# Performance work log

Measured on AMD Instinct MI355X. Metric: run time of the kernel, lower is better.

## Reference

```python
import jax, jax.numpy as jnp
import numpy as np

B, C, W, H, HID = 8, 512, 64, 32, 256
G = 5 * HID  # gates: i, f_left, f_up, o, candidate
EPS = 1e-5


def setup_inputs() -> dict:
    key = jax.random.key(0)
    ks = jax.random.split(key, 7)
    s_in = 1.0 / np.sqrt(C)
    s_h = 1.0 / np.sqrt(HID)
    return {
        "x": jax.random.normal(ks[0], (B, C, W, H), dtype=jnp.float32),
        "Wx": jax.random.normal(ks[1], (C, G), dtype=jnp.float32) * s_in,
        "Wh1": jax.random.normal(ks[2], (HID, G), dtype=jnp.float32) * s_h,  # left neighbor
        "Wh2": jax.random.normal(ks[3], (HID, G), dtype=jnp.float32) * s_h,  # up neighbor
        "b": jnp.zeros((G,), dtype=jnp.float32),
        "gamma": jnp.ones((HID,), dtype=jnp.float32),
        "beta": jnp.zeros((HID,), dtype=jnp.float32),
    }


def mdlstm(x, Wx, Wh1, Wh2, b):
    # x: (B, C, W, H). Precompute input projection once (big GEMM).
    xp = jnp.einsum('bcwh,cg->whbg', x, Wx) + b  # (W, H, B, G)
    z = jnp.zeros((B, HID), x.dtype)
    zrow = jnp.zeros((H, B, HID), x.dtype)

    def col_step(carry, inp):
        h_l, c_l = carry                 # left-neighbor state/cell (B, HID)
        xg, h_u, c_u = inp               # precomputed input gates + up-neighbor
        g = xg + h_l @ Wh1 + h_u @ Wh2   # (B, G)
        i, f1, f2, o, cand = jnp.split(g, 5, axis=-1)
        i = jax.nn.sigmoid(i)
        f1 = jax.nn.sigmoid(f1)
        f2 = jax.nn.sigmoid(f2)
        o = jax.nn.sigmoid(o)
        c = i * jnp.tanh(cand) + f1 * c_l + f2 * c_u
        h = o * jnp.tanh(c)
        return (h, c), (h, c)

    def row_step(prev, xp_w):
        h_up_row, c_up_row = prev        # previous width-row, each (H, B, HID)
        _, (h_row, c_row) = jax.lax.scan(col_step, (z, z), (xp_w, h_up_row, c_up_row))
        return (h_row, c_row), (h_row, c_row)

    _, (h_all, c_all) = jax.lax.scan(row_step, (zrow, zrow), xp)  # (W, H, B, HID)
    state = jnp.transpose(h_all, (2, 3, 0, 1))  # (B, HID, W, H)
    cell = jnp.transpose(c_all, (2, 3, 0, 1))
    return state, cell


def reference(x, Wx, Wh1, Wh2, b, gamma, beta):
    state, cell = mdlstm(x, Wx, Wh1, Wh2, b)
    # BatchNorm2d (training-mode batch statistics) over (N, W, H) per channel
    mean = state.mean(axis=(0, 2, 3), keepdims=True)
    var = state.var(axis=(0, 2, 3), keepdims=True)
    xn = (state - mean) * jax.lax.rsqrt(var + EPS)
    out = jnp.tanh(xn * gamma[None, :, None, None] + beta[None, :, None, None])
    return (out, (state, cell))
```

## Files before the change

kernel.cpp:

```cpp
#include <hip/hip_runtime.h>
#include <math.h>

#define B_ 8
#define C_ 512
#define W_ 64
#define H_ 32
#define HID_ 256
#define G_ 1280
#define WH_ (W_*H_)
#define CELL_STRIDE (B_*HID_)
#define SENT 0xFFFFFFFFu

typedef float v4f __attribute__((ext_vector_type(4)));

__device__ __forceinline__ float sigmoidf_(float x) {
    return 1.0f / (1.0f + __expf(-x));
}

__device__ __forceinline__ float tanhf_(float x) {
    float ax = fabsf(x);
    float e = __expf(-2.0f * ax);
    float t = (1.0f - e) / (1.0f + e);
    return copysignf(t, x);
}

__device__ __forceinline__ void stg_byp1(float* p, float v) {
    asm volatile("global_store_dword %0, %1, off sc0 sc1" :: "v"(p), "v"(v) : "memory");
}
__device__ __forceinline__ void ldg2_byp(const unsigned* p0, const unsigned* p1,
                                         unsigned& a, unsigned& b) {
    asm volatile("global_load_dword %0, %2, off sc0 sc1\n\t"
                 "global_load_dword %1, %3, off sc0 sc1\n\t"
                 "s_waitcnt vmcnt(0)"
                 : "=&v"(a), "=&v"(b)
                 : "v"(p0), "v"(p1)
                 : "memory");
}

__device__ __forceinline__ bool ok4(v4f v) {
    return (__float_as_uint(v.x) != SENT) & (__float_as_uint(v.y) != SENT) &
           (__float_as_uint(v.z) != SENT) & (__float_as_uint(v.w) != SENT);
}

__global__ __launch_bounds__(256) void k_transpose_x(const float* __restrict__ x,
                                                     float* __restrict__ xT) {
    __shared__ float tile[64][65];
    int bc0 = blockIdx.x * 64;
    int wh0 = blockIdx.y * 64;
    int xcol = threadIdx.x & 63;
    int yrow = threadIdx.x >> 6;
    for (int yy = yrow; yy < 64; yy += 4)
        tile[yy][xcol] = x[(size_t)(bc0 + yy) * WH_ + wh0 + xcol];
    __syncthreads();
    for (int yy = yrow; yy < 64; yy += 4)
        xT[(size_t)(wh0 + yy) * (B_*C_) + bc0 + xcol] = tile[xcol][yy];
}

#define BM 64
#define BN 128
#define BK 32
#define AS_STRIDE 68
#define BS_STRIDE 132

__global__ __launch_bounds__(256) void k_xproj(const float* __restrict__ xT,
                                               const float* __restrict__ Wx,
                                               const float* __restrict__ bias,
                                               float* __restrict__ xp) {
    __shared__ float As[BK * AS_STRIDE];
    __shared__ float Bs[BK * BS_STRIDE];

    int bid = blockIdx.x;
    int xcd = bid & 7;
    int slot = bid >> 3;
    int mt = xcd * 32 + slot / 10;
    int nt = slot % 10;
    int m0 = mt * BM, n0 = nt * BN;
    int tid = threadIdx.x;

    int tm  = (tid >> 5) * 8;
    int tn4 = (tid & 31) * 4;

    float4 acc[8];
#pragma unroll
    for (int i = 0; i < 8; ++i) { acc[i].x = acc[i].y = acc[i].z = acc[i].w = 0.f; }

    int ar = tid >> 2, aq = tid & 3;
    int br = tid >> 3, bq = tid & 7;

    for (int kc = 0; kc < C_; kc += BK) {
        float4 av0 = *(const float4*)(xT + (size_t)(m0 + ar) * C_ + kc + aq * 4);
        float4 av1 = *(const float4*)(xT + (size_t)(m0 + ar) * C_ + kc + (aq + 4) * 4);
        float4 bv[4];
#pragma unroll
        for (int s = 0; s < 4; ++s)
            bv[s] = *(const float4*)(Wx + (size_t)(kc + br) * G_ + n0 + (bq + 8 * s) * 4);

        __syncthreads();
        As[(aq * 4 + 0) * AS_STRIDE + ar] = av0.x;
        As[(aq * 4 + 1) * AS_STRIDE + ar] = av0.y;
        As[(aq * 4 + 2) * AS_STRIDE + ar] = av0.z;
        As[(aq * 4 + 3) * AS_STRIDE + ar] = av0.w;
        As[((aq + 4) * 4 + 0) * AS_STRIDE + ar] = av1.x;
        As[((aq + 4) * 4 + 1) * AS_STRIDE + ar] = av1.y;
        As[((aq + 4) * 4 + 2) * AS_STRIDE + ar] = av1.z;
        As[((aq + 4) * 4 + 3) * AS_STRIDE + ar] = av1.w;
#pragma unroll
        for (int s = 0; s < 4; ++s)
            *(float4*)&Bs[br * BS_STRIDE + (bq + 8 * s) * 4] = bv[s];
        __syncthreads();

#pragma unroll
        for (int k = 0; k < BK; ++k) {
            float4 a0 = *(const float4*)&As[k * AS_STRIDE + tm];
            float4 a1 = *(const float4*)&As[k * AS_STRIDE + tm + 4];
            float4 b0 = *(const float4*)&Bs[k * BS_STRIDE + tn4];
            float am[8] = {a0.x, a0.y, a0.z, a0.w, a1.x, a1.y, a1.z, a1.w};
#pragma unroll
            for (int i = 0; i < 8; ++i) {
                acc[i].x += am[i] * b0.x;
                acc[i].y += am[i] * b0.y;
                acc[i].z += am[i] * b0.z;
                acc[i].w += am[i] * b0.w;
            }
        }
    }

    float4 bb = *(const float4*)(bias + n0 + tn4);
#pragma unroll
    for (int i = 0; i < 8; ++i) {
        float4 o;
        o.x = acc[i].x + bb.x; o.y = acc[i].y + bb.y;
        o.z = acc[i].z + bb.z; o.w = acc[i].w + bb.w;
        *(float4*)(xp + (size_t)(m0 + tm + i) * G_ + n0 + tn4) = o;
    }
}

#define NT 32
#define NWV 8
#define GPS (NWV*160 + 8)

__global__ __launch_bounds__(512, 2) void k_scan(const float* __restrict__ xp,
                                                 const float* __restrict__ Wh1,
                                                 const float* __restrict__ Wh2,
                                                 float* __restrict__ hbuf,
                                                 float* __restrict__ cbuf) {
    __shared__ float hs[2][B_ * HID_];
    __shared__ float gp[B_ * GPS];

    int w0b = blockIdx.x >> 3;
    int nt  = blockIdx.x & 7;
    int n0  = nt * NT;
    int tid = threadIdx.x;

    int kq  = tid >> 5;
    int c0  = tid & 31;
    int sel = kq >> 3;
    int kk0 = (kq & 7) * 32;
    const float* Wm = sel ? Wh2 : Wh1;
    const float* hbase = &hs[sel][0];
    int wv = tid >> 6;
    bool lo32 = (tid & 63) < 32;

    float wr[5][32];
#pragma unroll
    for (int g = 0; g < 5; ++g)
#pragma unroll
        for (int k = 0; k < 32; ++k)
            wr[g][k] = Wm[(size_t)(kk0 + k) * G_ + g * 256 + n0 + c0];

    int b2 = tid >> 5, nn2 = tid & 31;
    bool cok = (tid < 256);
    int xob = b2 * G_ + n0 + nn2;
    int co  = b2 * HID_ + n0 + nn2;
    int gr  = b2 * GPS + nn2;
    int gwb = wv * 160 + c0;

    for (int rr = 0; rr < 2; ++rr) {
        int w = w0b + rr * 32;
        float creg = 0.f;
        for (int h = 0; h < H_; ++h) {
            int wh = w * H_ + h;

            float xpre[5];
            if (cok) {
                const float* xrow = xp + (size_t)wh * (B_ * G_) + xob;
#pragma unroll
                for (int g = 0; g < 5; ++g) xpre[g] = xrow[g * 256];
            }

            bool vl = (h > 0), vu = (w > 0);
            const float* pl = vl ? hbuf + (size_t)(wh - 1)  * CELL_STRIDE + tid * 4 : hbuf;
            const float* pu = vu ? hbuf + (size_t)(wh - H_) * CELL_STRIDE + tid * 4 : hbuf;
            const float* pc = (vu && cok) ? cbuf + (size_t)(wh - H_) * CELL_STRIDE + co : cbuf;

            if ((tid & 63) == 0) {
                if (vl | vu) {
                    for (;;) {
                        unsigned a, bvv;
                        ldg2_byp((const unsigned*)pl, (const unsigned*)pu, a, bvv);
                        if ((((!vl)) | (a != SENT)) & (((!vu)) | (bvv != SENT))) break;
                        __builtin_amdgcn_s_sleep(2);
                    }
                }
            }

            v4f l0 = {0.f, 0.f, 0.f, 0.f};
            v4f u0 = {0.f, 0.f, 0.f, 0.f};
            float cu = 0.f;
            bool needl = vl, needu = vu, needc = vu && cok;
            for (;;) {
                v4f tl, tu; float tc;
                asm volatile(
                    "global_load_dwordx4 %0, %3, off sc0 sc1\n\t"
                    "global_load_dwordx4 %1, %4, off sc0 sc1\n\t"
                    "global_load_dword %2, %5, off sc0 sc1\n\t"
                    "s_waitcnt vmcnt(0)"
                    : "=&v"(tl), "=&v"(tu), "=&v"(tc)
                    : "v"(pl), "v"(pu), "v"(pc)
                    : "memory");
                if (needl & ok4(tl)) { l0 = tl; needl = false; }
                if (needu & ok4(tu)) { u0 = tu; needu = false; }
                if (needc & (__float_as_uint(tc) != SENT)) { cu = tc; needc = false; }
                if (__ballot(needl | needu | needc) == 0) break;
                __builtin_amdgcn_s_sleep(1);
            }
            ((v4f*)hs[0])[tid] = l0;
            ((v4f*)hs[1])[tid] = u0;
            __syncthreads();

            float acc[5][8];
#pragma unroll
            for (int g = 0; g < 5; ++g)
#pragma unroll
                for (int b = 0; b < 8; ++b) acc[g][b] = 0.f;

#pragma unroll
            for (int k4 = 0; k4 < 8; ++k4) {
#pragma unroll
                for (int b = 0; b < 8; ++b) {
                    float4 hv = *(const float4*)&hbase[b * HID_ + kk0 + k4 * 4];
#pragma unroll
                    for (int g = 0; g < 5; ++g) {
                        acc[g][b] += hv.x * wr[g][k4 * 4 + 0];
                        acc[g][b] += hv.y * wr[g][k4 * 4 + 1];
                        acc[g][b] += hv.z * wr[g][k4 * 4 + 2];
                        acc[g][b] += hv.w * wr[g][k4 * 4 + 3];
                    }
                }
            }

#pragma unroll
            for (int v = 0; v < 20; ++v) {
                const int ia = v, ib = v + 20;
                float xa = acc[ia >> 3][ia & 7], ya = xa;
                float xb = acc[ib >> 3][ib & 7], yb = xb;
                asm("v_permlane32_swap_b32 %0, %1" : "+v"(xa), "+v"(ya));
                asm("v_permlane32_swap_b32 %0, %1" : "+v"(xb), "+v"(yb));
                float sa = xa + ya;
                float sb = xb + yb;
                float val = lo32 ? sa : sb;
                const int offA = (ia & 7) * GPS + (ia >> 3) * 32;
                const int offB = (ib & 7) * GPS + (ib >> 3) * 32;
                gp[gwb + (lo32 ? offA : offB)] = val;
            }
            __syncthreads();

            if (cok) {
                float gv[5];
#pragma unroll
                for (int g = 0; g < 5; ++g) {
                    float s = xpre[g];
#pragma unroll
                    for (int q = 0; q < NWV; ++q)
                        s += gp[gr + q * 160 + g * 32];
                    gv[g] = s;
                }
                float iv = sigmoidf_(gv[0]);
                float f1 = sigmoidf_(gv[1]);
                float f2 = sigmoidf_(gv[2]);
                float ov = sigmoidf_(gv[3]);
                float cd = tanhf_(gv[4]);
                float cv = iv * cd + f1 * creg + f2 * cu;
                float hh = ov * tanhf_(cv);
                creg = cv;
                stg_byp1(cbuf + (size_t)wh * CELL_STRIDE + co, cv);
                stg_byp1(hbuf + (size_t)wh * CELL_STRIDE + co, hh);
            }
        }
    }
}

__global__ __launch_bounds__(256) void k_stats(const float* __restrict__ hbuf,
                                               float* __restrict__ ssum,
                                               float* __restrict__ ssq) {
    int t = threadIdx.x;
    size_t r0 = (size_t)blockIdx.x * 64;
    float s = 0.f, q = 0.f;
    for (int r = 0; r < 64; ++r) {
        float v = hbuf[(r0 + r) * HID_ + t];
        s += v; q += v * v;
    }
    atomicAdd(&ssum[t], s);
    atomicAdd(&ssq[t], q);
}

__global__ void k_finstats(const float* __restrict__ ssum, const float* __restrict__ ssq,
                           float* __restrict__ mean, float* __restrict__ rinv) {
    int t = threadIdx.x;
    const float inv_n = 1.0f / 16384.0f;
    float m = ssum[t] * inv_n;
    float v = ssq[t] * inv_n - m * m;
    mean[t] = m;
    rinv[t] = rsqrtf(v + 1e-5f);
}

__global__ __launch_bounds__(256) void k_out(const float* __restrict__ hbuf,
                                             const float* __restrict__ cbuf,
                                             const float* __restrict__ mean,
                                             const float* __restrict__ rinv,
                                             const float* __restrict__ gamma,
                                             const float* __restrict__ beta,
                                             float* __restrict__ outp) {
    __shared__ float tile[64][65];
    int bi = blockIdx.x;
    int b = bi >> 7;
    int rem = bi & 127;
    int wh0 = (rem >> 2) * 64;
    int n0 = (rem & 3) * 64;
    int xcol = threadIdx.x & 63;
    int yrow = threadIdx.x >> 6;

    float* out0   = outp;
    float* state0 = outp + (size_t)B_ * HID_ * WH_;
    float* cell0  = state0 + (size_t)B_ * HID_ * WH_;

    for (int yy = yrow; yy < 64; yy += 4)
        tile[yy][xcol] = hbuf[((size_t)(wh0 + yy) * B_ + b) * HID_ + n0 + xcol];
    __syncthreads();
    for (int yy = yrow; yy < 64; yy += 4) {
        int n = n0 + yy;
        float sv = tile[xcol][yy];
        size_t oidx = ((size_t)b * HID_ + n) * WH_ + wh0 + xcol;
        state0[oidx] = sv;
        float xn = (sv - mean[n]) * rinv[n];
        out0[oidx] = tanhf_(xn * gamma[n] + beta[n]);
    }
    __syncthreads();

    for (int yy = yrow; yy < 64; yy += 4)
        tile[yy][xcol] = cbuf[((size_t)(wh0 + yy) * B_ + b) * HID_ + n0 + xcol];
    __syncthreads();

    for (int yy = yrow; yy < 64; yy += 4) {
        int n = n0 + yy;
        size_t oidx = ((size_t)b * HID_ + n) * WH_ + wh0 + xcol;
        cell0[oidx] = tile[xcol][yy];
    }
}

extern "C" void kernel_launch(void* const* d_in, const int* in_sizes, int n_in,
                              void* d_out, int out_size, void* d_ws, size_t ws_size,
                              hipStream_t stream) {
    const float* x     = (const float*)d_in[0];
    const float* Wx    = (const float*)d_in[1];
    const float* Wh1   = (const float*)d_in[2];
    const float* Wh2   = (const float*)d_in[3];
    const float* bias  = (const float*)d_in[4];
    const float* gamma = (const float*)d_in[5];
    const float* beta  = (const float*)d_in[6];
    float* out = (float*)d_out;
    float* ws  = (float*)d_ws;

    float* xp   = ws;
    float* xT   = ws + 20971520;
    float* hbuf = xT;
    float* cbuf = xT + 4194304;
    float* ssum = ws + 29360128;
    float* ssq  = ssum + 256;
    float* mean = ssum + 512;
    float* rinv = ssum + 768;

    k_transpose_x<<<dim3(64, 32), 256, 0, stream>>>(x, xT);
    k_xproj<<<2560, 256, 0, stream>>>(xT, Wx, bias, xp);

    hipMemsetAsync(ssum, 0, 1024 * sizeof(float), stream);
    hipMemsetAsync(hbuf, 0xFF, (size_t)8388608 * sizeof(float), stream);

    k_scan<<<256, 512, 0, stream>>>(xp, Wh1, Wh2, hbuf, cbuf);

    k_stats<<<256, 256, 0, stream>>>(hbuf, ssum, ssq);
    k_finstats<<<1, 256, 0, stream>>>(ssum, ssq, mean, rinv);
    k_out<<<8 * 32 * 4, 256, 0, stream>>>(hbuf, cbuf, mean, rinv, gamma, beta, out);
}
```

Before: 1.025 ms.

## Run input projection GEMM on bf16 MFMA with split-precision hi/lo operands

```diff
diff --git a/kernel.cpp b/kernel.cpp
--- a/kernel.cpp
+++ b/kernel.cpp
@@ -12,6 +12,8 @@
 #define SENT 0xFFFFFFFFu
 
 typedef float v4f __attribute__((ext_vector_type(4)));
+typedef __attribute__((ext_vector_type(8))) short bf16x8;
+typedef __attribute__((ext_vector_type(4))) float f32x4;
 
 __device__ __forceinline__ float sigmoidf_(float x) {
     return 1.0f / (1.0f + __expf(-x));
@@ -22,6 +24,15 @@
     float e = __expf(-2.0f * ax);
     float t = (1.0f - e) / (1.0f + e);
     return copysignf(t, x);
+}
+
+__device__ __forceinline__ unsigned short f2bf(float f) {
+    unsigned u = __float_as_uint(f);
+    u = u + 0x7FFFu + ((u >> 16) & 1u);
+    return (unsigned short)(u >> 16);
+}
+__device__ __forceinline__ float bf2f(unsigned short h) {
+    return __uint_as_float(((unsigned)h) << 16);
 }
 
 __device__ __forceinline__ void stg_byp1(float* p, float v) {
@@ -43,7 +54,8 @@
 }
 
 __global__ __launch_bounds__(256) void k_transpose_x(const float* __restrict__ x,
-                                                     float* __restrict__ xT) {
+                                                     unsigned short* __restrict__ xTh,
+                                                     unsigned short* __restrict__ xTl) {
     __shared__ float tile[64][65];
     int bc0 = blockIdx.x * 64;
     int wh0 = blockIdx.y * 64;
@@ -52,86 +64,129 @@
     for (int yy = yrow; yy < 64; yy += 4)
         tile[yy][xcol] = x[(size_t)(bc0 + yy) * WH_ + wh0 + xcol];
     __syncthreads();
+    for (int yy = yrow; yy < 64; yy += 4) {
+        float v = tile[xcol][yy];
+        unsigned short hi = f2bf(v);
+        unsigned short lo = f2bf(v - bf2f(hi));
+        size_t idx = (size_t)(wh0 + yy) * (B_*C_) + bc0 + xcol;
+        xTh[idx] = hi;
+        xTl[idx] = lo;
+    }
+}
+
+__global__ __launch_bounds__(256) void k_wxT(const float* __restrict__ Wx,
+                                             unsigned short* __restrict__ WxTh,
+                                             unsigned short* __restrict__ WxTl) {
+    __shared__ float tile[64][65];
+    int n0 = blockIdx.x * 64;
+    int k0 = blockIdx.y * 64;
+    int xcol = threadIdx.x & 63;
+    int yrow = threadIdx.x >> 6;
     for (int yy = yrow; yy < 64; yy += 4)
-        xT[(size_t)(wh0 + yy) * (B_*C_) + bc0 + xcol] = tile[xcol][yy];
-}
-
-#define BM 64
-#define BN 128
-#define BK 32
-#define AS_STRIDE 68
-#define BS_STRIDE 132
-
-__global__ __launch_bounds__(256) void k_xproj(const float* __restrict__ xT,
-                                               const float* __restrict__ Wx,
-                                               const float* __restrict__ bias,
-                                               float* __restrict__ xp) {
-    __shared__ float As[BK * AS_STRIDE];
-    __shared__ float Bs[BK * BS_STRIDE];
+        tile[yy][xcol] = Wx[(size_t)(k0 + yy) * G_ + n0 + xcol];
+    __syncthreads();
+    for (int yy = yrow; yy < 64; yy += 4) {
+        float v = tile[xcol][yy];
+        unsigned short hi = f2bf(v);
+        unsigned short lo = f2bf(v - bf2f(hi));
+        size_t idx = (size_t)(n0 + yy) * C_ + k0 + xcol;
+        WxTh[idx] = hi;
+        WxTl[idx] = lo;
+    }
+}
+
+#define XAS 40
+
+__global__ __launch_bounds__(256) void k_xproj_mfma(const unsigned short* __restrict__ xTh,
+                                                    const unsigned short* __restrict__ xTl,
+                                                    const unsigned short* __restrict__ WxTh,
+                                                    const unsigned short* __restrict__ WxTl,
+                                                    const float* __restrict__ bias,
+                                                    float* __restrict__ xp) {
+    __shared__ unsigned short Ash[128 * XAS];
+    __shared__ unsigned short Asl[128 * XAS];
+    __shared__ unsigned short Bsh[128 * XAS];
+    __shared__ unsigned short Bsl[128 * XAS];
 
     int bid = blockIdx.x;
-    int xcd = bid & 7;
-    int slot = bid >> 3;
-    int mt = xcd * 32 + slot / 10;
-    int nt = slot % 10;
-    int m0 = mt * BM, n0 = nt * BN;
+    int nt2 = bid % 10;
+    int mt  = bid / 10;
+    int m0 = mt * 128, n0 = nt2 * 128;
     int tid = threadIdx.x;
-
-    int tm  = (tid >> 5) * 8;
-    int tn4 = (tid & 31) * 4;
-
-    float4 acc[8];
-#pragma unroll
-    for (int i = 0; i < 8; ++i) { acc[i].x = acc[i].y = acc[i].z = acc[i].w = 0.f; }
-
-    int ar = tid >> 2, aq = tid & 3;
-    int br = tid >> 3, bq = tid & 7;
-
-    for (int kc = 0; kc < C_; kc += BK) {
-        float4 av0 = *(const float4*)(xT + (size_t)(m0 + ar) * C_ + kc + aq * 4);
-        float4 av1 = *(const float4*)(xT + (size_t)(m0 + ar) * C_ + kc + (aq + 4) * 4);
-        float4 bv[4];
-#pragma unroll
-        for (int s = 0; s < 4; ++s)
-            bv[s] = *(const float4*)(Wx + (size_t)(kc + br) * G_ + n0 + (bq + 8 * s) * 4);
-
+    int lane = tid & 63;
+    int wave = tid >> 6;
+    int wm = (wave >> 1) * 64;
+    int wn = (wave & 1) * 64;
+    int r16 = lane & 15;
+    int kg  = lane >> 4;
+
+    int srow = tid >> 1;
+    int sh   = (tid & 1) * 16;
+
+    f32x4 acc[4][4];
+#pragma unroll
+    for (int i = 0; i < 4; ++i)
+#pragma unroll
+        for (int j = 0; j < 4; ++j)
+            acc[i][j] = (f32x4)0.f;
+
+    const unsigned short* agh = xTh  + (size_t)(m0 + srow) * C_ + sh;
+    const unsigned short* agl = xTl  + (size_t)(m0 + srow) * C_ + sh;
+    const unsigned short* bgh = WxTh + (size_t)(n0 + srow) * C_ + sh;
+    const unsigned short* bgl = WxTl + (size_t)(n0 + srow) * C_ + sh;
+
+    for (int kc = 0; kc < C_; kc += 32) {
+        uint4 ah0 = *(const uint4*)(agh + kc);
+        uint4 ah1 = *(const uint4*)(agh + kc + 8);
+        uint4 al0 = *(const uint4*)(agl + kc);
+        uint4 al1 = *(const uint4*)(agl + kc + 8);
+        uint4 bh0 = *(const uint4*)(bgh + kc);
+        uint4 bh1 = *(const uint4*)(bgh + kc + 8);
+        uint4 bl0 = *(const uint4*)(bgl + kc);
+        uint4 bl1 = *(const uint4*)(bgl + kc + 8);
         __syncthreads();
-        As[(aq * 4 + 0) * AS_STRIDE + ar] = av0.x;
-        As[(aq * 4 + 1) * AS_STRIDE + ar] = av0.y;
-        As[(aq * 4 + 2) * AS_STRIDE + ar] = av0.z;
-        As[(aq * 4 + 3) * AS_STRIDE + ar] = av0.w;
-        As[((aq + 4) * 4 + 0) * AS_STRIDE + ar] = av1.x;
-        As[((aq + 4) * 4 + 1) * AS_STRIDE + ar] = av1.y;
-        As[((aq + 4) * 4 + 2) * AS_STRIDE + ar] = av1.z;
-        As[((aq + 4) * 4 + 3) * AS_STRIDE + ar] = av1.w;
-#pragma unroll
-        for (int s = 0; s < 4; ++s)
-            *(float4*)&Bs[br * BS_STRIDE + (bq + 8 * s) * 4] = bv[s];
+        *(uint4*)&Ash[srow * XAS + sh]     = ah0;
+        *(uint4*)&Ash[srow * XAS + sh + 8] = ah1;
+        *(uint4*)&Asl[srow * XAS + sh]     = al0;
+        *(uint4*)&Asl[srow * XAS + sh + 8] = al1;
+        *(uint4*)&Bsh[srow * XAS + sh]     = bh0;
+        *(uint4*)&Bsh[srow * XAS + sh + 8] = bh1;
+        *(uint4*)&Bsl[srow * XAS + sh]     = bl0;
+        *(uint4*)&Bsl[srow * XAS + sh + 8] = bl1;
         __syncthreads();
 
-#pragma unroll
-        for (int k = 0; k < BK; ++k) {
-            float4 a0 = *(const float4*)&As[k * AS_STRIDE + tm];
-            float4 a1 = *(const float4*)&As[k * AS_STRIDE + tm + 4];
-            float4 b0 = *(const float4*)&Bs[k * BS_STRIDE + tn4];
-            float am[8] = {a0.x, a0.y, a0.z, a0.w, a1.x, a1.y, a1.z, a1.w};
-#pragma unroll
-            for (int i = 0; i < 8; ++i) {
-                acc[i].x += am[i] * b0.x;
-                acc[i].y += am[i] * b0.y;
-                acc[i].z += am[i] * b0.z;
-                acc[i].w += am[i] * b0.w;
-            }
+        bf16x8 afh[4], afl[4], bfh[4], bfl[4];
+#pragma unroll
+        for (int i = 0; i < 4; ++i) {
+            afh[i] = *(const bf16x8*)&Ash[(wm + i * 16 + r16) * XAS + kg * 8];
+            afl[i] = *(const bf16x8*)&Asl[(wm + i * 16 + r16) * XAS + kg * 8];
         }
-    }
-
-    float4 bb = *(const float4*)(bias + n0 + tn4);
-#pragma unroll
-    for (int i = 0; i < 8; ++i) {
-        float4 o;
-        o.x = acc[i].x + bb.x; o.y = acc[i].y + bb.y;
-        o.z = acc[i].z + bb.z; o.w = acc[i].w + bb.w;
-        *(float4*)(xp + (size_t)(m0 + tm + i) * G_ + n0 + tn4) = o;
+#pragma unroll
+        for (int j = 0; j < 4; ++j) {
+            bfh[j] = *(const bf16x8*)&Bsh[(wn + j * 16 + r16) * XAS + kg * 8];
+            bfl[j] = *(const bf16x8*)&Bsl[(wn + j * 16 + r16) * XAS + kg * 8];
+        }
+#pragma unroll
+        for (int i = 0; i < 4; ++i)
+#pragma unroll
+            for (int j = 0; j < 4; ++j) {
+                acc[i][j] = __builtin_amdgcn_mfma_f32_16x16x32_bf16(afh[i], bfh[j], acc[i][j], 0, 0, 0);
+                acc[i][j] = __builtin_amdgcn_mfma_f32_16x16x32_bf16(afh[i], bfl[j], acc[i][j], 0, 0, 0);
+                acc[i][j] = __builtin_amdgcn_mfma_f32_16x16x32_bf16(afl[i], bfh[j], acc[i][j], 0, 0, 0);
+            }
+    }
+
+#pragma unroll
+    for (int j = 0; j < 4; ++j) {
+        int cb = n0 + wn + j * 16 + r16;
+        float bb = bias[cb];
+#pragma unroll
+        for (int i = 0; i < 4; ++i) {
+            int mb = m0 + wm + i * 16 + kg * 4;
+#pragma unroll
+            for (int q = 0; q < 4; ++q)
+                xp[(size_t)(mb + q) * G_ + cb] = acc[i][j][q] + bb;
+        }
     }
 }
 
@@ -372,16 +427,22 @@
     float* ws  = (float*)d_ws;
 
     float* xp   = ws;
-    float* xT   = ws + 20971520;
-    float* hbuf = xT;
-    float* cbuf = xT + 4194304;
+    float* hbuf = ws + 20971520;
+    float* cbuf = ws + 25165824;
     float* ssum = ws + 29360128;
     float* ssq  = ssum + 256;
     float* mean = ssum + 512;
     float* rinv = ssum + 768;
 
-    k_transpose_x<<<dim3(64, 32), 256, 0, stream>>>(x, xT);
-    k_xproj<<<2560, 256, 0, stream>>>(xT, Wx, bias, xp);
+    unsigned short* sb   = (unsigned short*)out;
+    unsigned short* xTh  = sb;
+    unsigned short* xTl  = sb + 8388608;
+    unsigned short* WxTh = sb + 16777216;
+    unsigned short* WxTl = sb + 17432576;
+
+    k_transpose_x<<<dim3(64, 32), 256, 0, stream>>>(x, xTh, xTl);
+    k_wxT<<<dim3(20, 8), 256, 0, stream>>>(Wx, WxTh, WxTl);
+    k_xproj_mfma<<<1280, 256, 0, stream>>>(xTh, xTl, WxTh, WxTl, bias, xp);
 
     hipMemsetAsync(ssum, 0, 1024 * sizeof(float), stream);
     hipMemsetAsync(hbuf, 0xFF, (size_t)8388608 * sizeof(float), stream);
```

After: 828.5 us. 1.24x faster.
